# Performance work log

Hardware: AMD Instinct MI355X
Metric: run time of the kernel (lower is better)

Reference implementation:

```python
import jax, jax.numpy as jnp
import numpy as np

D_MODEL = 1024
N_HEADS = 16
D_K = 64


def setup_inputs() -> dict:
    key = jax.random.key(0)
    ks = jax.random.split(key, 9)
    dkh = D_K * N_HEADS
    s = 1.0 / np.sqrt(D_MODEL)
    so = 1.0 / np.sqrt(dkh)
    return {
        "x": jax.random.normal(ks[0], (2, 2048, D_MODEL), dtype=jnp.float32),
        "Wq": jax.random.normal(ks[1], (D_MODEL, dkh), dtype=jnp.float32) * s,
        "bq": jnp.zeros((dkh,), dtype=jnp.float32),
        "Wk": jax.random.normal(ks[2], (D_MODEL, dkh), dtype=jnp.float32) * s,
        "bk": jnp.zeros((dkh,), dtype=jnp.float32),
        "Wv": jax.random.normal(ks[3], (D_MODEL, dkh), dtype=jnp.float32) * s,
        "bv": jnp.zeros((dkh,), dtype=jnp.float32),
        "Wo": jax.random.normal(ks[4], (dkh, D_MODEL), dtype=jnp.float32) * so,
        "bo": jnp.zeros((D_MODEL,), dtype=jnp.float32),
    }


def reference(x, Wq, bq, Wk, bk, Wv, bv, Wo, bo):
    B, S, _ = x.shape
    # project and split heads: [B, S, H, Dk] -> [B, H, S, Dk]
    def split(t):
        return t.reshape(B, S, N_HEADS, D_K).transpose(0, 2, 1, 3)
    q = split(x @ Wq + bq)
    k = split(x @ Wk + bk)
    v = split(x @ Wv + bv)
    scores = jnp.einsum("bhsd,bhtd->bhst", q, k) / jnp.sqrt(jnp.float32(D_K))
    weights = jax.nn.softmax(scores, axis=-1)
    out = jnp.einsum("bhst,bhtd->bhsd", weights, v)  # [B, H, S, Dk]
    out = out.transpose(0, 2, 1, 3).reshape(B, S, N_HEADS * D_K)
    return out @ Wo + bo
```

## Files before the change

### kernel.cpp

```cpp
#include <hip/hip_runtime.h>

typedef unsigned short u16;
typedef unsigned int u32;
typedef short bf16x4 __attribute__((ext_vector_type(4)));
typedef short bf16x8 __attribute__((ext_vector_type(8)));
typedef float f32x4 __attribute__((ext_vector_type(4)));
typedef u32 u32x2 __attribute__((ext_vector_type(2)));
typedef u32 u32x4 __attribute__((ext_vector_type(4)));

#define DEVINL __device__ __forceinline__

DEVINL u16 f2bf(float f) {
    u32 u = __builtin_bit_cast(u32, f);
    u32 r = u + 0x7fffu + ((u >> 16) & 1u);
    return (u16)(r >> 16);
}

DEVINL u32 pack2(float a, float b) {
    return (u32)f2bf(a) | ((u32)f2bf(b) << 16);
}

__global__ __launch_bounds__(256) void cast_x_kernel(const float4* __restrict__ in,
                                                     u16* __restrict__ outp) {
    int i = blockIdx.x * 256 + threadIdx.x;
    float4 v = in[i];
    ushort4 o;
    o.x = f2bf(v.x); o.y = f2bf(v.y); o.z = f2bf(v.z); o.w = f2bf(v.w);
    *(ushort4*)&outp[(size_t)i * 4] = o;
}

__global__ __launch_bounds__(256) void transpose_cast(
    const float* __restrict__ W0, const float* __restrict__ W1,
    const float* __restrict__ W2, const float* __restrict__ W3,
    u16* __restrict__ T0, u16* __restrict__ T1,
    u16* __restrict__ T2, u16* __restrict__ T3) {
    __shared__ __align__(16) u16 lds[64 * 68];
    int bid = blockIdx.x;
    const float* W; u16* T;
    switch (bid >> 8) {
        case 0:  W = W0; T = T0; break;
        case 1:  W = W1; T = T1; break;
        case 2:  W = W2; T = T2; break;
        default: W = W3; T = T3; break;
    }
    int tile = bid & 255;
    int k0 = (tile >> 4) << 6;
    int n0 = (tile & 15) << 6;
    int t = threadIdx.x;
    int rk = t >> 2;
    int cb = (t & 3) << 4;
#pragma unroll
    for (int j = 0; j < 4; ++j) {
        float4 v = *(const float4*)&W[(size_t)(k0 + rk) * 1024 + n0 + cb + 4 * j];
        ushort4 o;
        o.x = f2bf(v.x); o.y = f2bf(v.y); o.z = f2bf(v.z); o.w = f2bf(v.w);
        *(ushort4*)&lds[rk * 68 + cb + 4 * j] = o;
    }
    __syncthreads();
    int rn = t >> 2;
#pragma unroll
    for (int j2 = 0; j2 < 2; ++j2) {
        u16 tmp[8];
#pragma unroll
        for (int u = 0; u < 8; ++u)
            tmp[u] = lds[(cb + 8 * j2 + u) * 68 + rn];
        *(uint4*)&T[(size_t)(n0 + rn) * 1024 + k0 + cb + 8 * j2] = *(uint4*)tmp;
    }
}

template <int MODE>
__global__ __launch_bounds__(256) void gemm_kernel(
    const u16* __restrict__ A,
    const u16* __restrict__ W0t, const u16* __restrict__ W1t, const u16* __restrict__ W2t,
    const float* __restrict__ b0, const float* __restrict__ b1, const float* __restrict__ b2,
    u16* __restrict__ Oq, u16* __restrict__ Ok, u16* __restrict__ Ov,
    float* __restrict__ Fout) {
    constexpr int NB = (MODE == 0) ? 24 : 8;
    const int mb = blockIdx.x / NB, nb = blockIdx.x % NB;
    const int m0 = mb * 128, n0 = nb * 128;
    const int tid = threadIdx.x, lane = tid & 63, w = tid >> 6;
    const int wr = w >> 1, wc = w & 1;
    const int c = lane & 15, g = lane >> 4;

    __shared__ __align__(16) u16 Alds[128 * 64];
    __shared__ __align__(16) u16 Blds[128 * 64];

    const u16* Wt; const float* bias; int ncol0;
    if (MODE == 0) {
        const int tsel = n0 >> 10;
        Wt   = (tsel == 0) ? W0t : ((tsel == 1) ? W1t : W2t);
        bias = (tsel == 0) ? b0  : ((tsel == 1) ? b1  : b2);
        ncol0 = n0 & 1023;
    } else {
        Wt = W0t; bias = b0; ncol0 = n0;
    }

    const u16* Asrc = A  + (size_t)(m0    + 32 * w + (lane >> 3)) * 1024 + (lane & 7) * 8;
    const u16* Bsrc = Wt + (size_t)(ncol0 + 32 * w + (lane >> 3)) * 1024 + (lane & 7) * 8;
    u16* AldsW = &Alds[(32 * w) * 64];
    u16* BldsW = &Blds[(32 * w) * 64];

    f32x4 acc[4][4] = {};

    for (int kt = 0; kt < 16; ++kt) {
        const int k0 = kt * 64;
#pragma unroll
        for (int i = 0; i < 4; ++i) {
            __builtin_amdgcn_global_load_lds(
                (const __attribute__((address_space(1))) void*)(Asrc + k0 + i * 8 * 1024),
                (__attribute__((address_space(3))) void*)(AldsW + i * 8 * 64), 16, 0, 0);
            __builtin_amdgcn_global_load_lds(
                (const __attribute__((address_space(1))) void*)(Bsrc + k0 + i * 8 * 1024),
                (__attribute__((address_space(3))) void*)(BldsW + i * 8 * 64), 16, 0, 0);
        }
        __syncthreads();
#pragma unroll
        for (int kk = 0; kk < 2; ++kk) {
            bf16x8 af[4], bfr[4];
#pragma unroll
            for (int mf = 0; mf < 4; ++mf)
                af[mf] = *(const bf16x8*)&Alds[(c + 16 * mf + 64 * wr) * 64 + 8 * g + 32 * kk];
#pragma unroll
            for (int nf = 0; nf < 4; ++nf)
                bfr[nf] = *(const bf16x8*)&Blds[(c + 16 * nf + 64 * wc) * 64 + 8 * g + 32 * kk];
#pragma unroll
            for (int mf = 0; mf < 4; ++mf)
#pragma unroll
                for (int nf = 0; nf < 4; ++nf)
                    acc[mf][nf] = __builtin_amdgcn_mfma_f32_16x16x32_bf16(
                        af[mf], bfr[nf], acc[mf][nf], 0, 0, 0);
        }
        __syncthreads();
    }

    float biasv[4];
#pragma unroll
    for (int nf = 0; nf < 4; ++nf) biasv[nf] = bias[ncol0 + 64 * wc + 16 * nf + c];

    if (MODE == 0) {
        const int bi = m0 >> 11;
        const int tsel = n0 >> 10;
        if (tsel < 2) {
            u16* Odst = (tsel == 0) ? Oq : Ok;
#pragma unroll
            for (int nf = 0; nf < 4; ++nf) {
                const int n_in = ncol0 + 64 * wc + 16 * nf + c;
                const int h = n_in >> 6, d = n_in & 63;
                u16* base = Odst + ((size_t)(bi * 16 + h)) * 2048 * 64 + d;
#pragma unroll
                for (int mf = 0; mf < 4; ++mf)
#pragma unroll
                    for (int r = 0; r < 4; ++r) {
                        const int m = m0 + 64 * wr + 16 * mf + 4 * g + r;
                        const int s = m & 2047;
                        base[(size_t)s * 64] = f2bf(acc[mf][nf][r] + biasv[nf]);
                    }
            }
        } else {
#pragma unroll
            for (int nf = 0; nf < 4; ++nf) {
                const int n_in = ncol0 + 64 * wc + 16 * nf + c;
                const int h = n_in >> 6, d = n_in & 63;
                u16* base = Ov + ((size_t)((bi * 16 + h) * 64 + d)) * 2048;
#pragma unroll
                for (int mf = 0; mf < 4; ++mf) {
                    const int s = (m0 & 2047) + 64 * wr + 16 * mf + 4 * g;
                    u32x2 pr = {pack2(acc[mf][nf][0] + biasv[nf], acc[mf][nf][1] + biasv[nf]),
                                pack2(acc[mf][nf][2] + biasv[nf], acc[mf][nf][3] + biasv[nf])};
                    *(u32x2*)&base[s] = pr;
                }
            }
        }
    } else {
#pragma unroll
        for (int mf = 0; mf < 4; ++mf)
#pragma unroll
            for (int r = 0; r < 4; ++r) {
                const int m = m0 + 64 * wr + 16 * mf + 4 * g + r;
                float* rowp = Fout + (size_t)m * 1024 + n0 + 64 * wc;
#pragma unroll
                for (int nf = 0; nf < 4; ++nf)
                    rowp[16 * nf + c] = acc[mf][nf][r] + biasv[nf];
            }
    }
}

__global__ __launch_bounds__(256) void attn_kernel(
    const u16* __restrict__ Q, const u16* __restrict__ K, const u16* __restrict__ Vt,
    u16* __restrict__ O) {
    const int bid0 = blockIdx.x;
    const int bid = (bid0 & 7) * 64 + (bid0 >> 3);
    const int qb = bid & 15, h = (bid >> 4) & 15, b = bid >> 8;
    const int tid = threadIdx.x, lane = tid & 63, w = tid >> 6;
    const int c = lane & 15, g = lane >> 4;

    __shared__ __align__(16) u16 Klds[2][64 * 72];
    __shared__ __align__(16) u16 Vlds[2][64 * 72];

    const size_t hoff = ((size_t)(b * 16 + h)) * 2048 * 64;
    const u16* Qh = Q + hoff;
    const u16* Kh = K + hoff;
    const u16* Vh = Vt + hoff;

    const int qw = qb * 128 + w * 32;
    bf16x8 qf[2][2];
#pragma unroll
    for (int u = 0; u < 2; ++u)
#pragma unroll
        for (int kk = 0; kk < 2; ++kk)
            qf[u][kk] = *(const bf16x8*)&Qh[(size_t)(qw + 16 * u + c) * 64 + 8 * g + 32 * kk];

    f32x4 oacc[4][2] = {};
    float mrun[2] = {-3.0e38f, -3.0e38f}, lrun[2] = {0.f, 0.f};

    const int srow = tid >> 3;
    const int scol = (tid & 7) * 8;

    {
        uint4 ka = *(const uint4*)&Kh[(size_t)srow * 64 + scol];
        uint4 kb2 = *(const uint4*)&Kh[(size_t)(srow + 32) * 64 + scol];
        uint4 va = *(const uint4*)&Vh[(size_t)srow * 2048 + scol];
        uint4 vb = *(const uint4*)&Vh[(size_t)(srow + 32) * 2048 + scol];
        *(uint4*)&Klds[0][srow * 72 + scol] = ka;
        *(uint4*)&Klds[0][(srow + 32) * 72 + scol] = kb2;
        *(uint4*)&Vlds[0][srow * 72 + scol] = va;
        *(uint4*)&Vlds[0][(srow + 32) * 72 + scol] = vb;
    }
    __syncthreads();

    for (int kt = 0; kt < 32; ++kt) {
        const int cur = kt & 1, nxt = cur ^ 1;
        uint4 ka, kb2, va, vb;
        if (kt < 31) {
            ka  = *(const uint4*)&Kh[(size_t)((kt + 1) * 64 + srow) * 64 + scol];
            kb2 = *(const uint4*)&Kh[(size_t)((kt + 1) * 64 + srow + 32) * 64 + scol];
            va  = *(const uint4*)&Vh[(size_t)srow * 2048 + (kt + 1) * 64 + scol];
            vb  = *(const uint4*)&Vh[(size_t)(srow + 32) * 2048 + (kt + 1) * 64 + scol];
        }
        const u16* Kb0 = &Klds[cur][0];
        const u16* Vb0 = &Vlds[cur][0];

        f32x4 sacc[4][2] = {};
#pragma unroll
        for (int T = 0; T < 4; ++T)
#pragma unroll
            for (int kk = 0; kk < 2; ++kk) {
                bf16x8 kf = *(const bf16x8*)&Kb0[(16 * T + c) * 72 + 8 * g + 32 * kk];
#pragma unroll
                for (int u = 0; u < 2; ++u)
                    sacc[T][u] = __builtin_amdgcn_mfma_f32_16x16x32_bf16(
                        kf, qf[u][kk], sacc[T][u], 0, 0, 0);
            }

        float alpha[2];
#pragma unroll
        for (int u = 0; u < 2; ++u) {
            float mx = sacc[0][u][0];
#pragma unroll
            for (int T = 0; T < 4; ++T)
#pragma unroll
                for (int r = 0; r < 4; ++r) mx = fmaxf(mx, sacc[T][u][r]);
            mx = fmaxf(mx, __shfl_xor(mx, 16));
            mx = fmaxf(mx, __shfl_xor(mx, 32));
            const float mnew = fmaxf(mrun[u], mx * 0.125f);
            alpha[u] = __expf(mrun[u] - mnew);
            mrun[u] = mnew;
        }

        u32 pw[4][2][2];
        float lsum[2] = {0.f, 0.f};
#pragma unroll
        for (int T = 0; T < 4; ++T)
#pragma unroll
            for (int u = 0; u < 2; ++u) {
                float p0 = __expf(sacc[T][u][0] * 0.125f - mrun[u]);
                float p1 = __expf(sacc[T][u][1] * 0.125f - mrun[u]);
                float p2 = __expf(sacc[T][u][2] * 0.125f - mrun[u]);
                float p3 = __expf(sacc[T][u][3] * 0.125f - mrun[u]);
                lsum[u] += (p0 + p1) + (p2 + p3);
                pw[T][u][0] = pack2(p0, p1);
                pw[T][u][1] = pack2(p2, p3);
            }
#pragma unroll
        for (int u = 0; u < 2; ++u) {
            float s = lsum[u];
            s += __shfl_xor(s, 16);
            s += __shfl_xor(s, 32);
            lrun[u] = lrun[u] * alpha[u] + s;
#pragma unroll
            for (int dt = 0; dt < 4; ++dt)
#pragma unroll
                for (int r = 0; r < 4; ++r) oacc[dt][u][r] *= alpha[u];
        }

#pragma unroll
        for (int kb = 0; kb < 2; ++kb) {
            bf16x8 pf[2];
#pragma unroll
            for (int u = 0; u < 2; ++u) {
                u32x4 ww = {pw[2 * kb][u][0], pw[2 * kb][u][1],
                            pw[2 * kb + 1][u][0], pw[2 * kb + 1][u][1]};
                pf[u] = __builtin_bit_cast(bf16x8, ww);
            }
#pragma unroll
            for (int dt = 0; dt < 4; ++dt) {
                bf16x4 v0 = *(const bf16x4*)&Vb0[(16 * dt + c) * 72 + 32 * kb + 4 * g];
                bf16x4 v1 = *(const bf16x4*)&Vb0[(16 * dt + c) * 72 + 32 * kb + 16 + 4 * g];
                bf16x8 vf = __builtin_shufflevector(v0, v1, 0, 1, 2, 3, 4, 5, 6, 7);
#pragma unroll
                for (int u = 0; u < 2; ++u)
                    oacc[dt][u] = __builtin_amdgcn_mfma_f32_16x16x32_bf16(
                        vf, pf[u], oacc[dt][u], 0, 0, 0);
            }
        }

        if (kt < 31) {
            *(uint4*)&Klds[nxt][srow * 72 + scol] = ka;
            *(uint4*)&Klds[nxt][(srow + 32) * 72 + scol] = kb2;
            *(uint4*)&Vlds[nxt][srow * 72 + scol] = va;
            *(uint4*)&Vlds[nxt][(srow + 32) * 72 + scol] = vb;
        }
        __syncthreads();
    }

#pragma unroll
    for (int u = 0; u < 2; ++u) {
        const float inv = 1.0f / lrun[u];
        const size_t obase = ((size_t)(b * 2048 + qw + 16 * u + c)) * 1024 + h * 64 + 4 * g;
#pragma unroll
        for (int dt = 0; dt < 4; ++dt) {
            u32x2 pr = {pack2(oacc[dt][u][0] * inv, oacc[dt][u][1] * inv),
                        pack2(oacc[dt][u][2] * inv, oacc[dt][u][3] * inv)};
            *(u32x2*)&O[obase + 16 * dt] = pr;
        }
    }
}

extern "C" void kernel_launch(void* const* d_in, const int* in_sizes, int n_in,
                              void* d_out, int out_size, void* d_ws, size_t ws_size,
                              hipStream_t stream) {
    const float* x  = (const float*)d_in[0];
    const float* Wq = (const float*)d_in[1];
    const float* bq = (const float*)d_in[2];
    const float* Wk = (const float*)d_in[3];
    const float* bk = (const float*)d_in[4];
    const float* Wv = (const float*)d_in[5];
    const float* bv = (const float*)d_in[6];
    const float* Wo = (const float*)d_in[7];
    const float* bo = (const float*)d_in[8];
    float* out = (float*)d_out;

    if (ws_size < (size_t)51 * 1024 * 1024) return;

    u16* ws  = (u16*)d_ws;
    u16* xb  = ws;
    u16* wqt = xb  + 4096 * 1024;
    u16* wkt = wqt + 1024 * 1024;
    u16* wvt = wkt + 1024 * 1024;
    u16* wot = wvt + 1024 * 1024;
    u16* Qb  = wot + 1024 * 1024;
    u16* Kb  = Qb + 4194304;
    u16* Vtb = Kb + 4194304;
    u16* Ob  = Vtb + 4194304;

    cast_x_kernel<<<4096, 256, 0, stream>>>((const float4*)x, xb);
    transpose_cast<<<1024, 256, 0, stream>>>(Wq, Wk, Wv, Wo, wqt, wkt, wvt, wot);
    gemm_kernel<0><<<768, 256, 0, stream>>>(xb, wqt, wkt, wvt, bq, bk, bv,
                                            Qb, Kb, Vtb, nullptr);
    attn_kernel<<<512, 256, 0, stream>>>(Qb, Kb, Vtb, Ob);
    gemm_kernel<1><<<256, 256, 0, stream>>>(Ob, wot, nullptr, nullptr, bo, nullptr, nullptr,
                                            nullptr, nullptr, nullptr, out);
}
```

Before: 239.6 us.

## Halve attention query tile per block, fold softmax scale into Q, skip rescale

```diff
diff --git a/kernel.cpp b/kernel.cpp
--- a/kernel.cpp
+++ b/kernel.cpp
@@ -142,6 +142,7 @@
         const int tsel = n0 >> 10;
         if (tsel < 2) {
             u16* Odst = (tsel == 0) ? Oq : Ok;
+            const float sc = (tsel == 0) ? 0.125f : 1.0f;
 #pragma unroll
             for (int nf = 0; nf < 4; ++nf) {
                 const int n_in = ncol0 + 64 * wc + 16 * nf + c;
@@ -153,7 +154,7 @@
                     for (int r = 0; r < 4; ++r) {
                         const int m = m0 + 64 * wr + 16 * mf + 4 * g + r;
                         const int s = m & 2047;
-                        base[(size_t)s * 64] = f2bf(acc[mf][nf][r] + biasv[nf]);
+                        base[(size_t)s * 64] = f2bf((acc[mf][nf][r] + biasv[nf]) * sc);
                     }
             }
         } else {
@@ -189,8 +190,8 @@
     const u16* __restrict__ Q, const u16* __restrict__ K, const u16* __restrict__ Vt,
     u16* __restrict__ O) {
     const int bid0 = blockIdx.x;
-    const int bid = (bid0 & 7) * 64 + (bid0 >> 3);
-    const int qb = bid & 15, h = (bid >> 4) & 15, b = bid >> 8;
+    const int bid = (bid0 & 7) * 128 + (bid0 >> 3);
+    const int qb = bid & 31, h = (bid >> 5) & 15, b = bid >> 9;
     const int tid = threadIdx.x, lane = tid & 63, w = tid >> 6;
     const int c = lane & 15, g = lane >> 4;
 
@@ -202,25 +203,23 @@
     const u16* Kh = K + hoff;
     const u16* Vh = Vt + hoff;
 
-    const int qw = qb * 128 + w * 32;
-    bf16x8 qf[2][2];
-#pragma unroll
-    for (int u = 0; u < 2; ++u)
-#pragma unroll
-        for (int kk = 0; kk < 2; ++kk)
-            qf[u][kk] = *(const bf16x8*)&Qh[(size_t)(qw + 16 * u + c) * 64 + 8 * g + 32 * kk];
-
-    f32x4 oacc[4][2] = {};
-    float mrun[2] = {-3.0e38f, -3.0e38f}, lrun[2] = {0.f, 0.f};
+    const int q = qb * 64 + w * 16 + c;
+    bf16x8 qf[2];
+#pragma unroll
+    for (int kk = 0; kk < 2; ++kk)
+        qf[kk] = *(const bf16x8*)&Qh[(size_t)q * 64 + 8 * g + 32 * kk];
+
+    f32x4 oacc[4] = {};
+    float mrun = -3.0e38f, lrun = 0.f;
 
     const int srow = tid >> 3;
     const int scol = (tid & 7) * 8;
 
     {
-        uint4 ka = *(const uint4*)&Kh[(size_t)srow * 64 + scol];
+        uint4 ka  = *(const uint4*)&Kh[(size_t)srow * 64 + scol];
         uint4 kb2 = *(const uint4*)&Kh[(size_t)(srow + 32) * 64 + scol];
-        uint4 va = *(const uint4*)&Vh[(size_t)srow * 2048 + scol];
-        uint4 vb = *(const uint4*)&Vh[(size_t)(srow + 32) * 2048 + scol];
+        uint4 va  = *(const uint4*)&Vh[(size_t)srow * 2048 + scol];
+        uint4 vb  = *(const uint4*)&Vh[(size_t)(srow + 32) * 2048 + scol];
         *(uint4*)&Klds[0][srow * 72 + scol] = ka;
         *(uint4*)&Klds[0][(srow + 32) * 72 + scol] = kb2;
         *(uint4*)&Vlds[0][srow * 72 + scol] = va;
@@ -240,77 +239,60 @@
         const u16* Kb0 = &Klds[cur][0];
         const u16* Vb0 = &Vlds[cur][0];
 
-        f32x4 sacc[4][2] = {};
+        f32x4 sacc[4] = {};
 #pragma unroll
         for (int T = 0; T < 4; ++T)
 #pragma unroll
             for (int kk = 0; kk < 2; ++kk) {
                 bf16x8 kf = *(const bf16x8*)&Kb0[(16 * T + c) * 72 + 8 * g + 32 * kk];
-#pragma unroll
-                for (int u = 0; u < 2; ++u)
-                    sacc[T][u] = __builtin_amdgcn_mfma_f32_16x16x32_bf16(
-                        kf, qf[u][kk], sacc[T][u], 0, 0, 0);
-            }
-
-        float alpha[2];
-#pragma unroll
-        for (int u = 0; u < 2; ++u) {
-            float mx = sacc[0][u][0];
-#pragma unroll
-            for (int T = 0; T < 4; ++T)
-#pragma unroll
-                for (int r = 0; r < 4; ++r) mx = fmaxf(mx, sacc[T][u][r]);
-            mx = fmaxf(mx, __shfl_xor(mx, 16));
-            mx = fmaxf(mx, __shfl_xor(mx, 32));
-            const float mnew = fmaxf(mrun[u], mx * 0.125f);
-            alpha[u] = __expf(mrun[u] - mnew);
-            mrun[u] = mnew;
-        }
-
-        u32 pw[4][2][2];
-        float lsum[2] = {0.f, 0.f};
-#pragma unroll
-        for (int T = 0; T < 4; ++T)
-#pragma unroll
-            for (int u = 0; u < 2; ++u) {
-                float p0 = __expf(sacc[T][u][0] * 0.125f - mrun[u]);
-                float p1 = __expf(sacc[T][u][1] * 0.125f - mrun[u]);
-                float p2 = __expf(sacc[T][u][2] * 0.125f - mrun[u]);
-                float p3 = __expf(sacc[T][u][3] * 0.125f - mrun[u]);
-                lsum[u] += (p0 + p1) + (p2 + p3);
-                pw[T][u][0] = pack2(p0, p1);
-                pw[T][u][1] = pack2(p2, p3);
-            }
-#pragma unroll
-        for (int u = 0; u < 2; ++u) {
-            float s = lsum[u];
-            s += __shfl_xor(s, 16);
-            s += __shfl_xor(s, 32);
-            lrun[u] = lrun[u] * alpha[u] + s;
+                sacc[T] = __builtin_amdgcn_mfma_f32_16x16x32_bf16(kf, qf[kk], sacc[T], 0, 0, 0);
+            }
+
+        float t0 = fmaxf(fmaxf(sacc[0][0], sacc[0][1]), fmaxf(sacc[0][2], sacc[0][3]));
+        float t1 = fmaxf(fmaxf(sacc[1][0], sacc[1][1]), fmaxf(sacc[1][2], sacc[1][3]));
+        float t2 = fmaxf(fmaxf(sacc[2][0], sacc[2][1]), fmaxf(sacc[2][2], sacc[2][3]));
+        float t3 = fmaxf(fmaxf(sacc[3][0], sacc[3][1]), fmaxf(sacc[3][2], sacc[3][3]));
+        float mx = fmaxf(fmaxf(t0, t1), fmaxf(t2, t3));
+        mx = fmaxf(mx, __shfl_xor(mx, 16));
+        mx = fmaxf(mx, __shfl_xor(mx, 32));
+
+        if (__any(mx > mrun)) {
+            const float mnew = fmaxf(mrun, mx);
+            const float alpha = __expf(mrun - mnew);
+            mrun = mnew;
+            lrun *= alpha;
 #pragma unroll
             for (int dt = 0; dt < 4; ++dt)
 #pragma unroll
-                for (int r = 0; r < 4; ++r) oacc[dt][u][r] *= alpha[u];
-        }
+                for (int r = 0; r < 4; ++r) oacc[dt][r] *= alpha;
+        }
+
+        u32 pw[4][2];
+        float lsum = 0.f;
+#pragma unroll
+        for (int T = 0; T < 4; ++T) {
+            float p0 = __expf(sacc[T][0] - mrun);
+            float p1 = __expf(sacc[T][1] - mrun);
+            float p2 = __expf(sacc[T][2] - mrun);
+            float p3 = __expf(sacc[T][3] - mrun);
+            lsum += (p0 + p1) + (p2 + p3);
+            pw[T][0] = pack2(p0, p1);
+            pw[T][1] = pack2(p2, p3);
+        }
+        lsum += __shfl_xor(lsum, 16);
+        lsum += __shfl_xor(lsum, 32);
+        lrun += lsum;
 
 #pragma unroll
         for (int kb = 0; kb < 2; ++kb) {
-            bf16x8 pf[2];
-#pragma unroll
-            for (int u = 0; u < 2; ++u) {
-                u32x4 ww = {pw[2 * kb][u][0], pw[2 * kb][u][1],
-                            pw[2 * kb + 1][u][0], pw[2 * kb + 1][u][1]};
-                pf[u] = __builtin_bit_cast(bf16x8, ww);
-            }
+            u32x4 ww = {pw[2 * kb][0], pw[2 * kb][1], pw[2 * kb + 1][0], pw[2 * kb + 1][1]};
+            bf16x8 pf = __builtin_bit_cast(bf16x8, ww);
 #pragma unroll
             for (int dt = 0; dt < 4; ++dt) {
                 bf16x4 v0 = *(const bf16x4*)&Vb0[(16 * dt + c) * 72 + 32 * kb + 4 * g];
                 bf16x4 v1 = *(const bf16x4*)&Vb0[(16 * dt + c) * 72 + 32 * kb + 16 + 4 * g];
                 bf16x8 vf = __builtin_shufflevector(v0, v1, 0, 1, 2, 3, 4, 5, 6, 7);
-#pragma unroll
-                for (int u = 0; u < 2; ++u)
-                    oacc[dt][u] = __builtin_amdgcn_mfma_f32_16x16x32_bf16(
-                        vf, pf[u], oacc[dt][u], 0, 0, 0);
+                oacc[dt] = __builtin_amdgcn_mfma_f32_16x16x32_bf16(vf, pf, oacc[dt], 0, 0, 0);
             }
         }
 
@@ -323,16 +305,13 @@
         __syncthreads();
     }
 
-#pragma unroll
-    for (int u = 0; u < 2; ++u) {
-        const float inv = 1.0f / lrun[u];
-        const size_t obase = ((size_t)(b * 2048 + qw + 16 * u + c)) * 1024 + h * 64 + 4 * g;
-#pragma unroll
-        for (int dt = 0; dt < 4; ++dt) {
-            u32x2 pr = {pack2(oacc[dt][u][0] * inv, oacc[dt][u][1] * inv),
-                        pack2(oacc[dt][u][2] * inv, oacc[dt][u][3] * inv)};
-            *(u32x2*)&O[obase + 16 * dt] = pr;
-        }
+    const float inv = 1.0f / lrun;
+    const size_t obase = ((size_t)(b * 2048 + q)) * 1024 + h * 64 + 4 * g;
+#pragma unroll
+    for (int dt = 0; dt < 4; ++dt) {
+        u32x2 pr = {pack2(oacc[dt][0] * inv, oacc[dt][1] * inv),
+                    pack2(oacc[dt][2] * inv, oacc[dt][3] * inv)};
+        *(u32x2*)&O[obase + 16 * dt] = pr;
     }
 }
 
@@ -367,7 +346,7 @@
     transpose_cast<<<1024, 256, 0, stream>>>(Wq, Wk, Wv, Wo, wqt, wkt, wvt, wot);
     gemm_kernel<0><<<768, 256, 0, stream>>>(xb, wqt, wkt, wvt, bq, bk, bv,
                                             Qb, Kb, Vtb, nullptr);
-    attn_kernel<<<512, 256, 0, stream>>>(Qb, Kb, Vtb, Ob);
+    attn_kernel<<<1024, 256, 0, stream>>>(Qb, Kb, Vtb, Ob);
     gemm_kernel<1><<<256, 256, 0, stream>>>(Ob, wot, nullptr, nullptr, bo, nullptr, nullptr,
                                             nullptr, nullptr, nullptr, out);
 }
```

Result: slower. 245.2 us (+2.3%).
